# Performance work log

Measured on AMD Instinct MI355X. Metric: run time of the kernel, lower is better.

Reference implementation:

```python
import jax, jax.numpy as jnp
import numpy as np

SCOPE = 63          # length of ricker inhibition filter (odd)
IN_CHANNELS = 256   # circulant matrix size == channel dim
SELF_CONNECT = False


def ricker(scope, width, damp, self_connect=False):
    # symmetric ricker (mexican-hat) wavelet of length `scope`, centered
    x = jnp.arange(scope, dtype=jnp.float32) - scope // 2
    w2 = width * width
    r = damp * (1.0 - x * x / w2) * jnp.exp(-x * x / (2.0 * w2))
    if not self_connect:
        r = r.at[scope // 2].set(0.0)  # no self-connection: zero center tap
    return r


def toeplitz1d_circular(f, size):
    # embed the centered length-`scope` filter into the first row of a
    # size x size circulant matrix (center tap on the diagonal, tails wrap)
    half = f.shape[0] // 2
    row0 = jnp.zeros(size, f.dtype)
    row0 = row0.at[: half + 1].set(f[half:])      # center + right tail
    row0 = row0.at[size - half:].set(f[:half])    # left tail wraps around
    idx = (jnp.arange(size)[:, None] - jnp.arange(size)[None, :]) % size
    return row0[idx]  # C[i, j] = row0[(i - j) mod size]


def setup_inputs() -> dict:
    key = jax.random.key(0)
    activations = jax.random.normal(key, (64, IN_CHANNELS, 56, 56), dtype=jnp.float32)
    damp = jnp.asarray(0.12, dtype=jnp.float32)   # learnable scalar
    width = jnp.asarray(3.0, dtype=jnp.float32)   # learnable scalar
    return {"activations": activations, "damp": damp, "width": width}


def reference(activations, damp, width):
    f = ricker(SCOPE, width, damp, SELF_CONNECT)
    tpl = toeplitz1d_circular(f, IN_CHANNELS)
    tpl_inv = jnp.linalg.inv(jnp.eye(IN_CHANNELS, dtype=f.dtype) - tpl)
    # apply inhibition matrix along the channel axis at every pixel
    return jnp.einsum('ij,bjhw->bihw', tpl_inv, activations)
```

## Files before the change

kernel.cpp:

```cpp
#include <hip/hip_runtime.h>


#define IN_CH 256
#define HW    3136
#define TP    64
#define KC    128

typedef __bf16 bf16x8 __attribute__((ext_vector_type(8)));
typedef float  f32x4  __attribute__((ext_vector_type(4)));

#define WS_AHI_OFF 1024
#define WS_ALO_OFF (1024 + 131072)

__global__ __launch_bounds__(256) void pi_build_m(const float* __restrict__ damp,
                                                  const float* __restrict__ width,
                                                  float* __restrict__ ws_m) {
    __shared__ float cS[256], gS[256], ctab[256];
    int t = threadIdx.x;
    float w = width[0], dmp = damp[0];

    ctab[t] = cosf((float)t * 0.0245436926f );

    int x = (t < 128) ? t : t - 256;
    float cv = 0.0f;
    if (t != 0 && x >= -31 && x <= 31) {
        float fx2 = (float)(x * x);
        float w2  = w * w;
        cv = dmp * (1.0f - fx2 / w2) * expf(-fx2 / (2.0f * w2));
    }
    cS[t] = cv;
    __syncthreads();

    float lam = 0.0f;
    for (int n = 0; n < 256; n++) lam += cS[n] * ctab[(t * n) & 255];
    gS[t] = 1.0f / (1.0f - lam);
    __syncthreads();

    float md = 0.0f;
    for (int k = 0; k < 256; k++) md += gS[k] * ctab[(t * k) & 255];
    ws_m[t] = md * (1.0f / 256.0f);
}

__global__ __launch_bounds__(256) void pi_build_afrag(const float* __restrict__ ws_m,
                                                      bf16x8* __restrict__ ahi,
                                                      bf16x8* __restrict__ alo) {
    int gid = blockIdx.x * 256 + threadIdx.x;
    int l = gid & 63;
    int t = (gid >> 6) & 15;
    int s = gid >> 10;
    int i = 16 * t + (l & 15);
    int kbase = 32 * s + 8 * (l >> 4);
    bf16x8 h, lo;
#pragma unroll
    for (int j = 0; j < 8; j++) {
        float v = ws_m[(i - (kbase + j)) & 255];
        __bf16 hb = (__bf16)v;
        h[j]  = hb;
        lo[j] = (__bf16)(v - (float)hb);
    }
    ahi[gid] = h;
    alo[gid] = lo;
}

__device__ __forceinline__ int lds_didx(int p, int jb) {
    int cb = (jb ^ (p & 15) ^ ((p >> 2) & 3) ^ ((p >> 4) & 3)) & 15;
    return p * 64 + cb * 4;
}

__global__ __launch_bounds__(256, 3) void pi_gemm(const float* __restrict__ act,
                                                  float* __restrict__ out,
                                                  const bf16x8* __restrict__ ahi,
                                                  const bf16x8* __restrict__ alo) {
    __shared__ __align__(16) unsigned int ldsHi[TP * KC / 2];
    __shared__ __align__(16) unsigned int ldsLo[TP * KC / 2];

    int tid  = threadIdx.x;
    int lane = tid & 63;
    int wv   = tid >> 6;

    int b    = blockIdx.x / 49;
    int tile = blockIdx.x - b * 49;
    int p0   = tile * TP;

    const float* actb = act + (size_t)b * (IN_CH * HW) + p0;
    float*       outb = out + (size_t)b * (IN_CH * HW) + p0;

    f32x4 acc[4][4] = {};

    int px4 = tid & 15;
    int jb  = tid >> 4;
    int pl  = px4 * 4;

    for (int c = 0; c < 2; c++) {
        {
            const float* src = actb + (size_t)(c * KC + jb * 8) * HW + pl;
            f32x4 v[8];
#pragma unroll
            for (int jj = 0; jj < 8; jj++)
                v[jj] = *(const f32x4*)(src + (size_t)jj * HW);
#pragma unroll
            for (int pp = 0; pp < 4; pp++) {
                int p = pl + pp;
                int didx = lds_didx(p, jb);
                bf16x8 hv, lv;
#pragma unroll
                for (int jj = 0; jj < 8; jj++) {
                    float xv = v[jj][pp];
                    __bf16 hb = (__bf16)xv;
                    hv[jj] = hb;
                    lv[jj] = (__bf16)(xv - (float)hb);
                }
                *(bf16x8*)(ldsHi + didx) = hv;
                *(bf16x8*)(ldsLo + didx) = lv;
            }
        }
        __syncthreads();

#pragma unroll
        for (int s = 0; s < 4; s++) {
            bf16x8 bh[4], bl[4];
#pragma unroll
            for (int ni = 0; ni < 4; ni++) {
                int p   = 16 * ni + (lane & 15);
                int jbb = 4 * s + (lane >> 4);
                int didx = lds_didx(p, jbb);
                bh[ni] = *(const bf16x8*)(ldsHi + didx);
                bl[ni] = *(const bf16x8*)(ldsLo + didx);
            }
            int sg = 4 * c + s;
#pragma unroll
            for (int ti = 0; ti < 4; ti++) {
                int t = 4 * wv + ti;
                int aidx = (sg * 16 + t) * 64 + lane;
                bf16x8 ah = ahi[aidx];
                bf16x8 al = alo[aidx];
#pragma unroll
                for (int ni = 0; ni < 4; ni++) {
                    acc[ti][ni] = __builtin_amdgcn_mfma_f32_16x16x32_bf16(ah, bh[ni], acc[ti][ni], 0, 0, 0);
                    acc[ti][ni] = __builtin_amdgcn_mfma_f32_16x16x32_bf16(ah, bl[ni], acc[ti][ni], 0, 0, 0);
                    acc[ti][ni] = __builtin_amdgcn_mfma_f32_16x16x32_bf16(al, bh[ni], acc[ti][ni], 0, 0, 0);
                }
            }
        }
        __syncthreads();
    }

    int col  = lane & 15;
    int rowq = (lane >> 4) * 4;
#pragma unroll
    for (int ti = 0; ti < 4; ti++) {
        int ibase = 64 * wv + 16 * ti + rowq;
#pragma unroll
        for (int ni = 0; ni < 4; ni++) {
            int p = 16 * ni + col;
#pragma unroll
            for (int r = 0; r < 4; r++) {
                outb[(size_t)(ibase + r) * HW + p] = acc[ti][ni][r];
            }
        }
    }
}

extern "C" void kernel_launch(void* const* d_in, const int* in_sizes, int n_in,
                              void* d_out, int out_size, void* d_ws, size_t ws_size,
                              hipStream_t stream) {
    const float* act   = (const float*)d_in[0];
    const float* damp  = (const float*)d_in[1];
    const float* width = (const float*)d_in[2];
    float* out = (float*)d_out;

    float*  ws_m = (float*)d_ws;
    bf16x8* ahi  = (bf16x8*)((char*)d_ws + WS_AHI_OFF);
    bf16x8* alo  = (bf16x8*)((char*)d_ws + WS_ALO_OFF);

    int batches = in_sizes[0] / (IN_CH * HW);

    pi_build_m<<<1, 256, 0, stream>>>(damp, width, ws_m);
    pi_build_afrag<<<32, 256, 0, stream>>>(ws_m, ahi, alo);
    pi_gemm<<<batches * 49, 256, 0, stream>>>(act, out, ahi, alo);
}
```

Measured before the change: 404.6 us.

## Replace split-bf16 three-pass MFMA with single-pass fp16 and merge setup kernels

Result: faster. 370.6 us (-8.4%).

```diff
diff --git a/kernel.cpp b/kernel.cpp
--- a/kernel.cpp
+++ b/kernel.cpp
@@ -6,16 +6,14 @@
 #define TP    64
 #define KC    128
 
-typedef __bf16 bf16x8 __attribute__((ext_vector_type(8)));
-typedef float  f32x4  __attribute__((ext_vector_type(4)));
+typedef _Float16 f16x8 __attribute__((ext_vector_type(8)));
+typedef float    f32x4 __attribute__((ext_vector_type(4)));
 
-#define WS_AHI_OFF 1024
-#define WS_ALO_OFF (1024 + 131072)
 
-__global__ __launch_bounds__(256) void pi_build_m(const float* __restrict__ damp,
-                                                  const float* __restrict__ width,
-                                                  float* __restrict__ ws_m) {
-    __shared__ float cS[256], gS[256], ctab[256];
+__global__ __launch_bounds__(256) void pi_build(const float* __restrict__ damp,
+                                                const float* __restrict__ width,
+                                                f16x8* __restrict__ afrag) {
+    __shared__ float cS[256], gS[256], ctab[256], mS[256];
     int t = threadIdx.x;
     float w = width[0], dmp = damp[0];
 
@@ -32,47 +30,42 @@
     __syncthreads();
 
     float lam = 0.0f;
+#pragma unroll 8
     for (int n = 0; n < 256; n++) lam += cS[n] * ctab[(t * n) & 255];
     gS[t] = 1.0f / (1.0f - lam);
     __syncthreads();
 
     float md = 0.0f;
+#pragma unroll 8
     for (int k = 0; k < 256; k++) md += gS[k] * ctab[(t * k) & 255];
-    ws_m[t] = md * (1.0f / 256.0f);
+    mS[t] = md * (1.0f / 256.0f);
+    __syncthreads();
+
+#pragma unroll
+    for (int g = 0; g < 32; g++) {
+        int gid = g * 256 + t;
+        int l  = gid & 63;
+        int tt = (gid >> 6) & 15;
+        int s  = gid >> 10;
+        int i     = 16 * tt + (l & 15);
+        int kbase = 32 * s + 8 * (l >> 4);
+        f16x8 h;
+#pragma unroll
+        for (int j = 0; j < 8; j++)
+            h[j] = (_Float16)mS[(i - (kbase + j)) & 255];
+        afrag[gid] = h;
+    }
 }
 
-__global__ __launch_bounds__(256) void pi_build_afrag(const float* __restrict__ ws_m,
-                                                      bf16x8* __restrict__ ahi,
-                                                      bf16x8* __restrict__ alo) {
-    int gid = blockIdx.x * 256 + threadIdx.x;
-    int l = gid & 63;
-    int t = (gid >> 6) & 15;
-    int s = gid >> 10;
-    int i = 16 * t + (l & 15);
-    int kbase = 32 * s + 8 * (l >> 4);
-    bf16x8 h, lo;
-#pragma unroll
-    for (int j = 0; j < 8; j++) {
-        float v = ws_m[(i - (kbase + j)) & 255];
-        __bf16 hb = (__bf16)v;
-        h[j]  = hb;
-        lo[j] = (__bf16)(v - (float)hb);
-    }
-    ahi[gid] = h;
-    alo[gid] = lo;
-}
-
-__device__ __forceinline__ int lds_didx(int p, int jb) {
-    int cb = (jb ^ (p & 15) ^ ((p >> 2) & 3) ^ ((p >> 4) & 3)) & 15;
+__device__ __forceinline__ int lds_didx(int p, int cb16) {
+    int cb = (cb16 ^ (p & 15) ^ ((p >> 2) & 3) ^ ((p >> 4) & 3)) & 15;
     return p * 64 + cb * 4;
 }
 
-__global__ __launch_bounds__(256, 3) void pi_gemm(const float* __restrict__ act,
+__global__ __launch_bounds__(256, 4) void pi_gemm(const float* __restrict__ act,
                                                   float* __restrict__ out,
-                                                  const bf16x8* __restrict__ ahi,
-                                                  const bf16x8* __restrict__ alo) {
-    __shared__ __align__(16) unsigned int ldsHi[TP * KC / 2];
-    __shared__ __align__(16) unsigned int ldsLo[TP * KC / 2];
+                                                  const f16x8* __restrict__ afrag) {
+    __shared__ __align__(16) unsigned int lds[TP * KC / 2];
 
     int tid  = threadIdx.x;
     int lane = tid & 63;
@@ -87,9 +80,8 @@
 
     f32x4 acc[4][4] = {};
 
-    int px4 = tid & 15;
-    int jb  = tid >> 4;
-    int pl  = px4 * 4;
+    int pl = 4 * (tid & 15);
+    int jb = tid >> 4;
 
     for (int c = 0; c < 2; c++) {
         {
@@ -102,44 +94,32 @@
             for (int pp = 0; pp < 4; pp++) {
                 int p = pl + pp;
                 int didx = lds_didx(p, jb);
-                bf16x8 hv, lv;
+                f16x8 hv;
 #pragma unroll
-                for (int jj = 0; jj < 8; jj++) {
-                    float xv = v[jj][pp];
-                    __bf16 hb = (__bf16)xv;
-                    hv[jj] = hb;
-                    lv[jj] = (__bf16)(xv - (float)hb);
-                }
-                *(bf16x8*)(ldsHi + didx) = hv;
-                *(bf16x8*)(ldsLo + didx) = lv;
+                for (int jj = 0; jj < 8; jj++)
+                    hv[jj] = (_Float16)v[jj][pp];
+                *(f16x8*)(lds + didx) = hv;
             }
         }
         __syncthreads();
 
 #pragma unroll
         for (int s = 0; s < 4; s++) {
-            bf16x8 bh[4], bl[4];
+            f16x8 bh[4];
 #pragma unroll
             for (int ni = 0; ni < 4; ni++) {
-                int p   = 16 * ni + (lane & 15);
-                int jbb = 4 * s + (lane >> 4);
-                int didx = lds_didx(p, jbb);
-                bh[ni] = *(const bf16x8*)(ldsHi + didx);
-                bl[ni] = *(const bf16x8*)(ldsLo + didx);
+                int p    = 16 * ni + (lane & 15);
+                int cb16 = 4 * s + (lane >> 4);
+                bh[ni] = *(const f16x8*)(lds + lds_didx(p, cb16));
             }
             int sg = 4 * c + s;
 #pragma unroll
             for (int ti = 0; ti < 4; ti++) {
                 int t = 4 * wv + ti;
-                int aidx = (sg * 16 + t) * 64 + lane;
-                bf16x8 ah = ahi[aidx];
-                bf16x8 al = alo[aidx];
+                f16x8 ah = afrag[(sg * 16 + t) * 64 + lane];
 #pragma unroll
-                for (int ni = 0; ni < 4; ni++) {
-                    acc[ti][ni] = __builtin_amdgcn_mfma_f32_16x16x32_bf16(ah, bh[ni], acc[ti][ni], 0, 0, 0);
-                    acc[ti][ni] = __builtin_amdgcn_mfma_f32_16x16x32_bf16(ah, bl[ni], acc[ti][ni], 0, 0, 0);
-                    acc[ti][ni] = __builtin_amdgcn_mfma_f32_16x16x32_bf16(al, bh[ni], acc[ti][ni], 0, 0, 0);
-                }
+                for (int ni = 0; ni < 4; ni++)
+                    acc[ti][ni] = __builtin_amdgcn_mfma_f32_16x16x32_f16(ah, bh[ni], acc[ti][ni], 0, 0, 0);
             }
         }
         __syncthreads();
@@ -154,9 +134,8 @@
         for (int ni = 0; ni < 4; ni++) {
             int p = 16 * ni + col;
 #pragma unroll
-            for (int r = 0; r < 4; r++) {
+            for (int r = 0; r < 4; r++)
                 outb[(size_t)(ibase + r) * HW + p] = acc[ti][ni][r];
-            }
         }
     }
 }
@@ -169,13 +148,9 @@
     const float* width = (const float*)d_in[2];
     float* out = (float*)d_out;
 
-    float*  ws_m = (float*)d_ws;
-    bf16x8* ahi  = (bf16x8*)((char*)d_ws + WS_AHI_OFF);
-    bf16x8* alo  = (bf16x8*)((char*)d_ws + WS_ALO_OFF);
-
+    f16x8* afrag = (f16x8*)d_ws;
     int batches = in_sizes[0] / (IN_CH * HW);
 
-    pi_build_m<<<1, 256, 0, stream>>>(damp, width, ws_m);
-    pi_build_afrag<<<32, 256, 0, stream>>>(ws_m, ahi, alo);
-    pi_gemm<<<batches * 49, 256, 0, stream>>>(act, out, ahi, alo);
+    pi_build<<<1, 256, 0, stream>>>(damp, width, afrag);
+    pi_gemm<<<batches * 49, 256, 0, stream>>>(act, out, afrag);
 }
```
